# Kernel optimization log

Hardware: AMD Instinct MI355X
Metric: run time of the kernel (lower is better)

Reference implementation:

```python
import jax, jax.numpy as jnp
import numpy as np

WINDOW_SIZE = 64
HIDDEN = 1024
N_INTER = min(HIDDEN // 2, 4 * WINDOW_SIZE)  # 256
STD_SQUARED = (WINDOW_SIZE / 2) ** 2  # 1024.0
S_LEN = 65536


def setup_inputs() -> dict:
    key = jax.random.key(0)
    k1, k2, k3, k4, k5, k6 = jax.random.split(key, 6)
    return {
        "source_hiddens": jax.random.normal(k1, (S_LEN, HIDDEN), dtype=jnp.float32),
        "target_hidden": jax.random.normal(k2, (1, HIDDEN), dtype=jnp.float32),
        "fc1_w": jax.random.normal(k3, (N_INTER, HIDDEN), dtype=jnp.float32) * 0.02,
        "fc1_b": jax.random.normal(k4, (N_INTER,), dtype=jnp.float32) * 0.02,
        "fc2_w": jax.random.normal(k5, (1, N_INTER), dtype=jnp.float32) * 0.02,
        "fc2_b": jax.random.normal(k6, (1,), dtype=jnp.float32) * 0.02,
        "source_sentence_length": S_LEN,
    }


def reference(source_hiddens, target_hidden, fc1_w, fc1_b, fc2_w, fc2_b,
              source_sentence_length):
    S = source_sentence_length  # python int
    h_s = source_hiddens        # [S, H]
    h_t = target_hidden         # [1, H]

    # window-position predictor MLP
    p = jnp.tanh(h_t @ fc1_w.T + fc1_b)                     # [1, N_INTER]
    p_t = S * jax.nn.sigmoid(p @ fc2_w.T + fc2_b)           # [1, 1]

    # data-dependent window bounds -> jit-safe boolean mask over positions
    w_start = jnp.clip(jnp.ceil(p_t - WINDOW_SIZE), 0, None)[0, 0]
    w_end = jnp.clip(jnp.floor(p_t + WINDOW_SIZE), None, S - 1)[0, 0]
    pos = jnp.arange(S, dtype=jnp.float32)
    mask = (pos >= w_start) & (pos <= w_end)                # [S]

    # gaussian-decay scalar (faithful to original: uses S, not positions)
    e_t = jnp.exp((S - p_t) / (2.0 * STD_SQUARED))          # [1, 1]

    # score + softmax over dim=1 (singleton axis -> all ones), faithful quirk
    scores = h_s @ h_t.reshape(HIDDEN, 1)                   # [S, 1]
    a = jax.nn.softmax(scores, axis=1)                      # [S, 1] == ones
    a = jnp.where(mask[:, None], a, 0.0) * e_t              # zero outside window

    c_t = a.reshape(1, -1) @ h_s                            # [1, H]
    return c_t
```

## Files before the change

kernel.cpp:

```cpp
#include <hip/hip_runtime.h>


#define HIDDEN      1024
#define N_INTER     256
#define WINDOWF     64.0f
#define A_BLOCKS    64
#define ROWS_PER_BLOCK (N_INTER / A_BLOCKS)
#define C_COL_BLOCKS 4
#define C_ROW_CHUNKS 8

__global__ __launch_bounds__(256) void ka_mlp(
    const float* __restrict__ ht, const float* __restrict__ fc1w,
    const float* __restrict__ fc1b, const float* __restrict__ fc2w,
    float* __restrict__ partials, float* __restrict__ out)
{
    __shared__ float sh_ht[HIDDEN];
    __shared__ float sh_w[4];
    const int tid = threadIdx.x;
    const int b   = blockIdx.x;

    for (int k = tid; k < HIDDEN; k += 256) sh_ht[k] = ht[k];
    if (b == 0) {
        for (int k = tid; k < HIDDEN; k += 256) out[k] = 0.0f;
    }
    __syncthreads();

    const int wave = tid >> 6;
    const int lane = tid & 63;
    const int r    = b * ROWS_PER_BLOCK + wave;
    const float* __restrict__ row = fc1w + (size_t)r * HIDDEN;

    float d = 0.0f;
    #pragma unroll
    for (int k = 0; k < HIDDEN / 64; ++k) {
        const int idx = lane + 64 * k;
        d += sh_ht[idx] * row[idx];
    }
    #pragma unroll
    for (int off = 32; off > 0; off >>= 1) d += __shfl_down(d, off);

    if (lane == 0) sh_w[wave] = tanhf(d + fc1b[r]) * fc2w[r];
    __syncthreads();
    if (tid == 0) partials[b] = sh_w[0] + sh_w[1] + sh_w[2] + sh_w[3];
}

__global__ __launch_bounds__(256) void kc_window(
    const float* __restrict__ hs, const float* __restrict__ partials,
    const float* __restrict__ fc2b, float* __restrict__ out, int S)
{
    __shared__ float sh_sc[3];
    if (threadIdx.x == 0) {
        float z = 0.0f;
        for (int i = 0; i < A_BLOCKS; ++i) z += partials[i];
        z += fc2b[0];
        const float sig = 1.0f / (1.0f + expf(-z));
        const float p_t = (float)S * sig;
        float wsf = ceilf(p_t - WINDOWF);  if (wsf < 0.0f) wsf = 0.0f;
        float wef = floorf(p_t + WINDOWF);
        const float smax = (float)(S - 1); if (wef > smax) wef = smax;
        const float e_t = expf(((float)S - p_t) * (1.0f / 2048.0f));
        sh_sc[0] = e_t; sh_sc[1] = wsf; sh_sc[2] = wef;
    }
    __syncthreads();

    const float e_t = sh_sc[0];
    const int wstart = (int)sh_sc[1];
    const int wend   = (int)sh_sc[2];
    if (wend < wstart) return;

    const int count = wend - wstart + 1;
    const int chunk = (count + C_ROW_CHUNKS - 1) / C_ROW_CHUNKS;
    const int r0 = wstart + (int)blockIdx.y * chunk;
    if (r0 > wend) return;
    int r1 = r0 + chunk - 1; if (r1 > wend) r1 = wend;

    const int col = (int)blockIdx.x * 256 + (int)threadIdx.x;
    float acc = 0.0f;
    for (int r = r0; r <= r1; ++r)
        acc += hs[(size_t)r * HIDDEN + col];

    atomicAdd(&out[col], e_t * acc);
}

extern "C" void kernel_launch(void* const* d_in, const int* in_sizes, int n_in,
                              void* d_out, int out_size, void* d_ws, size_t ws_size,
                              hipStream_t stream) {
    const float* hs   = (const float*)d_in[0];
    const float* ht   = (const float*)d_in[1];
    const float* fc1w = (const float*)d_in[2];
    const float* fc1b = (const float*)d_in[3];
    const float* fc2w = (const float*)d_in[4];
    const float* fc2b = (const float*)d_in[5];
    const int S = in_sizes[0] / HIDDEN;

    float* out      = (float*)d_out;
    float* partials = (float*)d_ws;

    ka_mlp<<<A_BLOCKS, 256, 0, stream>>>(ht, fc1w, fc1b, fc2w, partials, out);
    kc_window<<<dim3(C_COL_BLOCKS, C_ROW_CHUNKS), 256, 0, stream>>>(
        hs, partials, fc2b, out, S);
}
```

Before: 311.4 us.

## Fuse window-predictor MLP and windowed row sum into a single kernel

Merges the two launches into one four-block kernel. Each block recomputes the full 256-row fc1 MLP in shared memory, derives the window bounds, then sums the window rows for its 256 columns. The final result is written directly, which removes the output zeroing, the partials buffer, the atomics and one kernel launch. In exchange, each wave serially computes 64 dot products, the MLP work is repeated in all four blocks, and the row sum runs on only 4 blocks, so it loses row-chunk parallelism.

```diff
diff --git a/kernel.cpp b/kernel.cpp
--- a/kernel.cpp
+++ b/kernel.cpp
@@ -1,85 +1,63 @@
 #include <hip/hip_runtime.h>
 
 
-#define HIDDEN      1024
-#define N_INTER     256
-#define WINDOWF     64.0f
-#define A_BLOCKS    64
-#define ROWS_PER_BLOCK (N_INTER / A_BLOCKS)
-#define C_COL_BLOCKS 4
-#define C_ROW_CHUNKS 8
+#define HIDDEN   1024
+#define N_INTER  256
+#define WINDOWF  64.0f
 
-__global__ __launch_bounds__(256) void ka_mlp(
-    const float* __restrict__ ht, const float* __restrict__ fc1w,
-    const float* __restrict__ fc1b, const float* __restrict__ fc2w,
-    float* __restrict__ partials, float* __restrict__ out)
+__global__ __launch_bounds__(256) void fused_local_attn(
+    const float* __restrict__ hs, const float* __restrict__ ht,
+    const float* __restrict__ fc1w, const float* __restrict__ fc1b,
+    const float* __restrict__ fc2w, const float* __restrict__ fc2b,
+    float* __restrict__ out, int S)
 {
     __shared__ float sh_ht[HIDDEN];
-    __shared__ float sh_w[4];
+    __shared__ float sh_r[N_INTER];
+    __shared__ float sh_sc[3];
+
     const int tid = threadIdx.x;
-    const int b   = blockIdx.x;
-
     for (int k = tid; k < HIDDEN; k += 256) sh_ht[k] = ht[k];
-    if (b == 0) {
-        for (int k = tid; k < HIDDEN; k += 256) out[k] = 0.0f;
-    }
     __syncthreads();
 
     const int wave = tid >> 6;
     const int lane = tid & 63;
-    const int r    = b * ROWS_PER_BLOCK + wave;
-    const float* __restrict__ row = fc1w + (size_t)r * HIDDEN;
+    for (int j = 0; j < N_INTER / 4; ++j) {
+        const int r = wave * (N_INTER / 4) + j;
+        const float* __restrict__ row = fc1w + (size_t)r * HIDDEN;
+        float d = 0.0f;
+        #pragma unroll
+        for (int k = 0; k < HIDDEN / 64; ++k)
+            d += sh_ht[lane + 64 * k] * row[lane + 64 * k];
+        #pragma unroll
+        for (int off = 32; off > 0; off >>= 1) d += __shfl_down(d, off);
+        if (lane == 0) sh_r[r] = tanhf(d + fc1b[r]) * fc2w[r];
+    }
+    __syncthreads();
 
-    float d = 0.0f;
-    #pragma unroll
-    for (int k = 0; k < HIDDEN / 64; ++k) {
-        const int idx = lane + 64 * k;
-        d += sh_ht[idx] * row[idx];
-    }
-    #pragma unroll
-    for (int off = 32; off > 0; off >>= 1) d += __shfl_down(d, off);
-
-    if (lane == 0) sh_w[wave] = tanhf(d + fc1b[r]) * fc2w[r];
-    __syncthreads();
-    if (tid == 0) partials[b] = sh_w[0] + sh_w[1] + sh_w[2] + sh_w[3];
-}
-
-__global__ __launch_bounds__(256) void kc_window(
-    const float* __restrict__ hs, const float* __restrict__ partials,
-    const float* __restrict__ fc2b, float* __restrict__ out, int S)
-{
-    __shared__ float sh_sc[3];
-    if (threadIdx.x == 0) {
+    if (tid == 0) {
         float z = 0.0f;
-        for (int i = 0; i < A_BLOCKS; ++i) z += partials[i];
+        for (int i = 0; i < N_INTER; ++i) z += sh_r[i];
         z += fc2b[0];
         const float sig = 1.0f / (1.0f + expf(-z));
         const float p_t = (float)S * sig;
         float wsf = ceilf(p_t - WINDOWF);  if (wsf < 0.0f) wsf = 0.0f;
         float wef = floorf(p_t + WINDOWF);
         const float smax = (float)(S - 1); if (wef > smax) wef = smax;
-        const float e_t = expf(((float)S - p_t) * (1.0f / 2048.0f));
-        sh_sc[0] = e_t; sh_sc[1] = wsf; sh_sc[2] = wef;
+        sh_sc[0] = expf(((float)S - p_t) * (1.0f / 2048.0f));
+        sh_sc[1] = wsf; sh_sc[2] = wef;
     }
     __syncthreads();
 
     const float e_t = sh_sc[0];
     const int wstart = (int)sh_sc[1];
     const int wend   = (int)sh_sc[2];
-    if (wend < wstart) return;
 
-    const int count = wend - wstart + 1;
-    const int chunk = (count + C_ROW_CHUNKS - 1) / C_ROW_CHUNKS;
-    const int r0 = wstart + (int)blockIdx.y * chunk;
-    if (r0 > wend) return;
-    int r1 = r0 + chunk - 1; if (r1 > wend) r1 = wend;
-
-    const int col = (int)blockIdx.x * 256 + (int)threadIdx.x;
+    const int col = (int)blockIdx.x * 256 + tid;
     float acc = 0.0f;
-    for (int r = r0; r <= r1; ++r)
+    for (int r = wstart; r <= wend; ++r)
         acc += hs[(size_t)r * HIDDEN + col];
 
-    atomicAdd(&out[col], e_t * acc);
+    out[col] = e_t * acc;
 }
 
 extern "C" void kernel_launch(void* const* d_in, const int* in_sizes, int n_in,
@@ -93,10 +71,6 @@
     const float* fc2b = (const float*)d_in[5];
     const int S = in_sizes[0] / HIDDEN;
 
-    float* out      = (float*)d_out;
-    float* partials = (float*)d_ws;
-
-    ka_mlp<<<A_BLOCKS, 256, 0, stream>>>(ht, fc1w, fc1b, fc2w, partials, out);
-    kc_window<<<dim3(C_COL_BLOCKS, C_ROW_CHUNKS), 256, 0, stream>>>(
-        hs, partials, fc2b, out, S);
+    fused_local_attn<<<HIDDEN / 256, 256, 0, stream>>>(
+        hs, ht, fc1w, fc1b, fc2w, fc2b, (float*)d_out, S);
 }
```

Result: slower. 430.3 us (+38.2%).
